# Kernel tuning notes

Measured on AMD Instinct MI355X. Metric: run time of the kernel, lower is better.

The kernel has to match this reference:

```python
import jax, jax.numpy as jnp
import numpy as np


def setup_inputs() -> dict:
    key = jax.random.key(0)
    k1, k2, k3, k4 = jax.random.split(key, 4)
    B, h, w, z, C = 4, 16, 16, 16, 128
    Cq = C // 8
    x = jax.random.normal(k1, (B, h, w, z, C), dtype=jnp.float32)
    # 1x1x1 Conv3D kernels == per-voxel linear projections (he_normal scale)
    Wb = jax.random.normal(k2, (C, Cq), dtype=jnp.float32) * np.sqrt(2.0 / C)
    Wc = jax.random.normal(k3, (C, Cq), dtype=jnp.float32) * np.sqrt(2.0 / C)
    Wd = jax.random.normal(k4, (C, C), dtype=jnp.float32) * np.sqrt(2.0 / C)
    gamma = jnp.zeros((1,), dtype=jnp.float32)
    return {"x": x, "Wb": Wb, "Wc": Wc, "Wd": Wd, "gamma": gamma}


def reference(x, Wb, Wc, Wd, gamma):
    B, h, w, z, C = x.shape
    N = h * w * z
    # 1x1x1 convs = channel projections
    b = jnp.einsum('bhwzc,cf->bhwzf', x, Wb).reshape(B, N, -1)   # [B,N,C/8]
    c = jnp.einsum('bhwzc,cf->bhwzf', x, Wc).reshape(B, N, -1)   # [B,N,C/8]
    d = jnp.einsum('bhwzc,cf->bhwzf', x, Wd).reshape(B, N, C)    # [B,N,C]
    # full NxN attention scores, softmax over last axis (keras softmax default)
    scores = jnp.einsum('bnf,bmf->bnm', b, c)                    # [B,N,N]
    attn = jax.nn.softmax(scores, axis=-1)
    out = jnp.einsum('bnm,bmc->bnc', attn, d).reshape(B, h, w, z, C)
    return gamma * out + x
```

## Files before the change

kernel.cpp:

```cpp
#include <hip/hip_runtime.h>

#define NB     4
#define NN     4096
#define NC     128
#define NCQ    16
#define NROWS  (NB * NN)
#define NSLICE 8
#define NIT    (NN / 64 / NSLICE)

typedef __attribute__((ext_vector_type(8)))  __bf16 bf16x8;
typedef __attribute__((ext_vector_type(4)))  float  f32x4;
typedef __attribute__((ext_vector_type(16))) float  f32x16;

#define MFMA16(a,b,c) __builtin_amdgcn_mfma_f32_16x16x32_bf16((a),(b),(c),0,0,0)
#define MFMA32(a,b,c) __builtin_amdgcn_mfma_f32_32x32x16_bf16((a),(b),(c),0,0,0)
#define LOG2E 1.44269504f
#define SCH_BIAS 16248.66f

__device__ __forceinline__ f32x16 zero16() {
    f32x16 v;
    #pragma unroll
    for (int i = 0; i < 16; ++i) v[i] = 0.f;
    return v;
}


__global__ __launch_bounds__(256) void wpre_kernel(
    const float* __restrict__ Wb, const float* __restrict__ Wc,
    const float* __restrict__ Wd, __bf16* __restrict__ Wp)
{
    int idx = blockIdx.x * 256 + threadIdx.x;
    int oc = idx >> 7, ch = idx & 127;
    float v;
    if (oc < 16)      v = Wb[ch * 16 + oc];
    else if (oc < 32) v = Wc[ch * 16 + (oc - 16)];
    else              v = Wd[ch * 128 + (oc - 32)];
    Wp[idx] = (__bf16)v;
}

__global__ __launch_bounds__(256) void proj_kernel(
    const float* __restrict__ x,  const __bf16* __restrict__ Wp,
    __bf16* __restrict__ qswz, __bf16* __restrict__ kswz,
    __bf16* __restrict__ vswz)
{
    __shared__ __align__(16) __bf16 xsh[32 * 136];
    __shared__ __align__(16) float  osb[4][16 * 17];

    const int  t    = threadIdx.x;
    const int  lane = t & 63, w = t >> 6;
    const int  q16  = lane & 15, quad = lane >> 4;
    const long row0 = (long)blockIdx.x * 32;
    const int  batch = (int)(row0 >> 12);
    const int  nloc  = (int)(row0 & 4095);
    const int  rh   = w & 1;
    const int  og   = (w >> 1) * 5;

    #pragma unroll
    for (int i = 0; i < 4; ++i) {
        int idx = t + 256 * i;
        int r = idx >> 5, c4 = (idx & 31) * 4;
        float4 xv = *(const float4*)&x[(row0 + r) * NC + c4];
        union { __bf16 h[4]; uint2 u; } cv;
        cv.h[0] = (__bf16)xv.x; cv.h[1] = (__bf16)xv.y;
        cv.h[2] = (__bf16)xv.z; cv.h[3] = (__bf16)xv.w;
        *(uint2*)&xsh[r * 136 + c4] = cv.u;
    }
    __syncthreads();

    bf16x8 xf[4];
    #pragma unroll
    for (int kc = 0; kc < 4; ++kc)
        xf[kc] = *(const bf16x8*)&xsh[(rh * 16 + q16) * 136 + kc * 32 + quad * 8];

    const __bf16* wbase = Wp + (size_t)(og * 16 + q16) * 128 + quad * 8;
    bf16x8 wfb[4];
    #pragma unroll
    for (int kc = 0; kc < 4; ++kc)
        wfb[kc] = *(const bf16x8*)(wbase + kc * 32);

    float* osw = osb[w];
    #pragma unroll
    for (int oc_t = 0; oc_t < 5; ++oc_t) {
        const int oset = og + oc_t;
        bf16x8 wfc[4];
        #pragma unroll
        for (int kc = 0; kc < 4; ++kc) wfc[kc] = wfb[kc];
        if (oc_t < 4) {
            const __bf16* wn = wbase + (size_t)(oc_t + 1) * 2048;
            #pragma unroll
            for (int kc = 0; kc < 4; ++kc)
                wfb[kc] = *(const bf16x8*)(wn + kc * 32);
        }
        f32x4 acc = {0.f, 0.f, 0.f, 0.f};
        #pragma unroll
        for (int kc = 0; kc < 4; ++kc)
            acc = MFMA16(wfc[kc], xf[kc], acc);
        #pragma unroll
        for (int r = 0; r < 4; ++r)
            osw[(quad * 4 + r) * 17 + q16] = acc[r];

        if (oset >= 2) {
            int ch_l = lane & 15, lh_t = (lane >> 4) & 1, jh = lane >> 5;
            union { __bf16 h[4]; uint2 u; } cv;
            #pragma unroll
            for (int u2 = 0; u2 < 4; ++u2)
                cv.h[u2] = (__bf16)osw[ch_l * 17 + 8 * jh + 4 * lh_t + u2];
            int kb16 = (nloc >> 4) + rh;
            int cg   = (oset - 2) >> 1;
            int l31v = ((oset - 2) & 1) * 16 + ch_l;
            size_t off = ((((size_t)batch * 256 + kb16) * 4 + cg) << 9)
                       + (size_t)(lh_t * 32 + l31v) * 8 + jh * 4;
            *(uint2*)&vswz[off] = cv.u;
        } else if (lane < 32) {
            int xr = lane & 15, lh_t = lane >> 4;
            const float qsc = (oset == 0) ? LOG2E : 1.f;
            union { __bf16 h[8]; uint4 u; } cv;
            #pragma unroll
            for (int j = 0; j < 8; ++j)
                cv.h[j] = (__bf16)(osw[(8 * lh_t + j) * 17 + xr] * qsc);
            size_t off = ((((size_t)batch * 128 + (nloc >> 5)) * 64)
                       + (size_t)(lh_t * 32 + rh * 16 + xr)) * 8;
            __bf16* dst = (oset == 0) ? qswz : kswz;
            *(uint4*)&dst[off] = cv.u;
        }
    }
}

__global__ __launch_bounds__(256, 4) void attn_kernel(
    const __bf16* __restrict__ qswz, const __bf16* __restrict__ kswz,
    const __bf16* __restrict__ vswz, __bf16* __restrict__ Opart,
    float* __restrict__ lws)
{
    const int t    = threadIdx.x;
    const int lane = t & 63, w = t >> 6;
    const int l31 = lane & 31, lh = lane >> 5;
    const int bid   = blockIdx.x;
    const int xcd   = bid & 7;
    const int batch = xcd >> 1;
    const int spL   = xcd & 1;
    const int idx   = bid >> 3;
    const int qpair = idx & 63;
    const int spH   = idx >> 6;
    const int slice = (spH << 1) | spL;
    const int qb32  = qpair * 2 + (w >> 1);
    const int h     = w & 1;
    const int ks0   = slice * (64 * NIT);

    const bf16x8 qf = *(const bf16x8*)
        &qswz[(((size_t)batch * 128 + qb32) * 64 + lane) * 8];

    const __bf16* kptr = kswz + ((size_t)batch * 128 + (ks0 >> 5)) * 512 + lane * 8;
    const __bf16* vptr = vswz + ((size_t)batch * 256 + (ks0 >> 4)) * 2048
                       + h * 1024 + lane * 8;

    union { uint32_t u[4]; bf16x8 f; } onesu;
    #pragma unroll
    for (int i = 0; i < 4; ++i) onesu.u[i] = 0x3F803F80u;
    const bf16x8 ones = onesu.f;

    f32x16 O0 = zero16(), O1 = zero16(), Ol = zero16();

    bf16x8 kf0 = *(const bf16x8*)(kptr);
    bf16x8 kf1 = *(const bf16x8*)(kptr + 512);
    bf16x8 va[8], vb[8];
    #pragma unroll
    for (int b = 0; b < 4; ++b) {
        va[2*b]     = *(const bf16x8*)(vptr + (size_t)(b * 4)     * 512);
        va[2*b + 1] = *(const bf16x8*)(vptr + (size_t)(b * 4 + 1) * 512);
    }
    f32x16 S0 = MFMA32(kf0, qf, zero16());
    f32x16 S1 = MFMA32(kf1, qf, zero16());

#define ATTN_BODY(IT, CUR, NXT)                                               \
    {                                                                         \
        const int itn = ((IT) + 1 < NIT) ? (IT) + 1 : (IT);                   \
        kf0 = *(const bf16x8*)(kptr + (size_t)itn * 1024);                    \
        kf1 = *(const bf16x8*)(kptr + (size_t)itn * 1024 + 512);              \
        _Pragma("unroll")                                                     \
        for (int b = 0; b < 4; ++b) {                                         \
            NXT[2*b]     = *(const bf16x8*)(vptr + (size_t)((itn*4+b)*4)*512);\
            NXT[2*b + 1] = *(const bf16x8*)(vptr + (size_t)((itn*4+b)*4+1)*512);\
        }                                                                     \
        union { uint32_t u32[16]; bf16x8 f[4]; } pk;                          \
        _Pragma("unroll")                                                     \
        for (int i = 0; i < 8; ++i) {                                         \
            int e0 = (int)fmaf(S0[2*i],   128.f, SCH_BIAS);                   \
            int e1 = (int)fmaf(S0[2*i+1], 128.f, SCH_BIAS);                   \
            int e2 = (int)fmaf(S1[2*i],   128.f, SCH_BIAS);                   \
            int e3 = (int)fmaf(S1[2*i+1], 128.f, SCH_BIAS);                   \
            pk.u32[i]     = (uint32_t)((e1 << 16) | e0);                      \
            pk.u32[8 + i] = (uint32_t)((e3 << 16) | e2);                      \
        }                                                                     \
        _Pragma("unroll")                                                     \
        for (int b = 0; b < 4; ++b) {                                         \
            O0 = MFMA32(pk.f[b], CUR[2*b],     O0);                           \
            O1 = MFMA32(pk.f[b], CUR[2*b + 1], O1);                           \
            Ol = MFMA32(pk.f[b], ones,         Ol);                           \
        }                                                                     \
        S0 = MFMA32(kf0, qf, zero16());                                       \
        S1 = MFMA32(kf1, qf, zero16());                                       \
    }

    for (int it = 0; it < NIT; it += 2) {
        ATTN_BODY(it,     va, vb);
        ATTN_BODY(it + 1, vb, va);
    }
#undef ATTN_BODY

    const long base = (long)batch * NN;

    if (h == 0 && l31 == 0) {
        #pragma unroll
        for (int r = 0; r < 16; ++r) {
            int q = qb32 * 32 + (r & 3) + 8 * (r >> 2) + 4 * lh;
            lws[(size_t)slice * NROWS + base + q] = Ol[r];
        }
    }

    #pragma unroll
    for (int ct = 0; ct < 2; ++ct) {
        f32x16 Ov = ct ? O1 : O0;
        #pragma unroll
        for (int r = 0; r < 16; ++r) {
            int q = qb32 * 32 + (r & 3) + 8 * (r >> 2) + 4 * lh;
            Opart[((size_t)slice * NROWS + base + q) * NC + 64 * h + 32 * ct + l31]
                = (__bf16)Ov[r];
        }
    }
}

__global__ __launch_bounds__(256) void combine_kernel(
    const __bf16* __restrict__ Op, const float* __restrict__ lws,
    const float* __restrict__ x, const float* __restrict__ gamma,
    float* __restrict__ out)
{
    __shared__ float gl[32];
    const int  t    = threadIdx.x;
    const long row0 = (long)blockIdx.x * 32;
    if (t < 32) {
        float l = 0.f;
        #pragma unroll
        for (int s = 0; s < NSLICE; ++s) l += lws[(size_t)s * NROWS + row0 + t];
        gl[t] = gamma[0] / l;
    }
    __syncthreads();
    const size_t s1 = (size_t)NROWS * NC;
    #pragma unroll
    for (int i = 0; i < 2; ++i) {
        int idx = t + 256 * i;
        int r = idx >> 4, c8 = (idx & 15) * 8;
        size_t g = (size_t)(row0 + r) * NC + c8;
        float a[8];
        #pragma unroll
        for (int j = 0; j < 8; ++j) a[j] = 0.f;
        #pragma unroll
        for (int s = 0; s < NSLICE; ++s) {
            union { __bf16 h[8]; uint4 u; } av;
            av.u = *(const uint4*)&Op[s1 * s + g];
            #pragma unroll
            for (int j = 0; j < 8; ++j) a[j] += (float)av.h[j];
        }
        float sc = gl[r];
        float4 x0 = *(const float4*)&x[g];
        float4 x1 = *(const float4*)&x[g + 4];
        float4 o0, o1;
        o0.x = a[0] * sc + x0.x; o0.y = a[1] * sc + x0.y;
        o0.z = a[2] * sc + x0.z; o0.w = a[3] * sc + x0.w;
        o1.x = a[4] * sc + x1.x; o1.y = a[5] * sc + x1.y;
        o1.z = a[6] * sc + x1.z; o1.w = a[7] * sc + x1.w;
        *(float4*)&out[g]     = o0;
        *(float4*)&out[g + 4] = o1;
    }
}

extern "C" void kernel_launch(void* const* d_in, const int* in_sizes, int n_in,
                              void* d_out, int out_size, void* d_ws, size_t ws_size,
                              hipStream_t stream) {
    const float* x     = (const float*)d_in[0];
    const float* Wb    = (const float*)d_in[1];
    const float* Wc    = (const float*)d_in[2];
    const float* Wd    = (const float*)d_in[3];
    const float* gamma = (const float*)d_in[4];
    float*       out   = (float*)d_out;

    __bf16* qswz  = (__bf16*)d_ws;
    __bf16* kswz  = qswz + (size_t)NROWS * NCQ;
    __bf16* vswz  = kswz + (size_t)NROWS * NCQ;
    __bf16* Opart = vswz + (size_t)NB * NC * NN;
    float*  lws   = (float*)(Opart + (size_t)NSLICE * NROWS * NC);
    __bf16* Wp    = (__bf16*)(lws + (size_t)NSLICE * NROWS);

    wpre_kernel   <<<80, 256, 0, stream>>>(Wb, Wc, Wd, Wp);
    proj_kernel   <<<NROWS / 32, 256, 0, stream>>>(x, Wp, qswz, kswz, vswz);
    attn_kernel   <<<NB * 128 * 4, 256, 0, stream>>>(qswz, kswz, vswz, Opart, lws);
    combine_kernel<<<NROWS / 32, 256, 0, stream>>>(Opart, lws, x, gamma, out);
}
```

Baseline: 129.8 us.

## Halve key slices, compute row sums on VALU, stage partial outputs through LDS

The key dimension is now split into 4 slices instead of 8, which halves the grid and the partial-output and row-sum traffic that the combine kernel has to read. The row-sum MFMA against a ones vector is replaced by a scalar accumulation of the bf16-cast exponentials plus a cross-half shuffle. That removes one of every three PV-stage MFMAs. Partial outputs are transposed through shared memory so each block writes them as coalesced 16-byte stores, and the loop is fully unrolled. In exchange, V is no longer prefetched one iteration ahead, so load latency may be exposed, and fewer blocks give less parallelism across the GPU.

```diff
diff --git a/kernel.cpp b/kernel.cpp
--- a/kernel.cpp
+++ b/kernel.cpp
@@ -5,7 +5,7 @@
 #define NC     128
 #define NCQ    16
 #define NROWS  (NB * NN)
-#define NSLICE 8
+#define NSLICE 4
 #define NIT    (NN / 64 / NSLICE)
 
 typedef __attribute__((ext_vector_type(8)))  __bf16 bf16x8;
@@ -131,6 +131,8 @@
     const __bf16* __restrict__ vswz, __bf16* __restrict__ Opart,
     float* __restrict__ lws)
 {
+    __shared__ __align__(16) __bf16 osh[64 * 136];
+
     const int t    = threadIdx.x;
     const int lane = t & 63, w = t >> 6;
     const int l31 = lane & 31, lh = lane >> 5;
@@ -153,33 +155,25 @@
     const __bf16* vptr = vswz + ((size_t)batch * 256 + (ks0 >> 4)) * 2048
                        + h * 1024 + lane * 8;
 
-    union { uint32_t u[4]; bf16x8 f; } onesu;
-    #pragma unroll
-    for (int i = 0; i < 4; ++i) onesu.u[i] = 0x3F803F80u;
-    const bf16x8 ones = onesu.f;
-
-    f32x16 O0 = zero16(), O1 = zero16(), Ol = zero16();
+    f32x16 O0 = zero16(), O1 = zero16();
+    float  lacc = 0.f;
+    const bool do_l = (h == 0);
 
     bf16x8 kf0 = *(const bf16x8*)(kptr);
     bf16x8 kf1 = *(const bf16x8*)(kptr + 512);
-    bf16x8 va[8], vb[8];
-    #pragma unroll
-    for (int b = 0; b < 4; ++b) {
-        va[2*b]     = *(const bf16x8*)(vptr + (size_t)(b * 4)     * 512);
-        va[2*b + 1] = *(const bf16x8*)(vptr + (size_t)(b * 4 + 1) * 512);
-    }
     f32x16 S0 = MFMA32(kf0, qf, zero16());
     f32x16 S1 = MFMA32(kf1, qf, zero16());
 
-#define ATTN_BODY(IT, CUR, NXT)                                               \
+#define ATTN_BODY(IT)                                                         \
     {                                                                         \
         const int itn = ((IT) + 1 < NIT) ? (IT) + 1 : (IT);                   \
         kf0 = *(const bf16x8*)(kptr + (size_t)itn * 1024);                    \
         kf1 = *(const bf16x8*)(kptr + (size_t)itn * 1024 + 512);              \
+        bf16x8 va[8];                                                         \
         _Pragma("unroll")                                                     \
         for (int b = 0; b < 4; ++b) {                                         \
-            NXT[2*b]     = *(const bf16x8*)(vptr + (size_t)((itn*4+b)*4)*512);\
-            NXT[2*b + 1] = *(const bf16x8*)(vptr + (size_t)((itn*4+b)*4+1)*512);\
+            va[2*b]   = *(const bf16x8*)(vptr + (size_t)(((IT)*4+b)*4)*512);  \
+            va[2*b+1] = *(const bf16x8*)(vptr + (size_t)(((IT)*4+b)*4+1)*512);\
         }                                                                     \
         union { uint32_t u32[16]; bf16x8 f[4]; } pk;                          \
         _Pragma("unroll")                                                     \
@@ -190,42 +184,54 @@
             int e3 = (int)fmaf(S1[2*i+1], 128.f, SCH_BIAS);                   \
             pk.u32[i]     = (uint32_t)((e1 << 16) | e0);                      \
             pk.u32[8 + i] = (uint32_t)((e3 << 16) | e2);                      \
+            if (do_l) {                                                       \
+                union { uint32_t u; float fv; } c0, c1, c2, c3;               \
+                c0.u = (uint32_t)e0 << 16; c1.u = (uint32_t)e1 << 16;         \
+                c2.u = (uint32_t)e2 << 16; c3.u = (uint32_t)e3 << 16;         \
+                lacc += (c0.fv + c1.fv) + (c2.fv + c3.fv);                    \
+            }                                                                 \
         }                                                                     \
         _Pragma("unroll")                                                     \
         for (int b = 0; b < 4; ++b) {                                         \
-            O0 = MFMA32(pk.f[b], CUR[2*b],     O0);                           \
-            O1 = MFMA32(pk.f[b], CUR[2*b + 1], O1);                           \
-            Ol = MFMA32(pk.f[b], ones,         Ol);                           \
+            O0 = MFMA32(pk.f[b], va[2*b],     O0);                            \
+            O1 = MFMA32(pk.f[b], va[2*b + 1], O1);                            \
         }                                                                     \
         S0 = MFMA32(kf0, qf, zero16());                                       \
         S1 = MFMA32(kf1, qf, zero16());                                       \
     }
 
+    #pragma unroll
     for (int it = 0; it < NIT; it += 2) {
-        ATTN_BODY(it,     va, vb);
-        ATTN_BODY(it + 1, vb, va);
+        ATTN_BODY(it);
+        ATTN_BODY(it + 1);
     }
 #undef ATTN_BODY
 
     const long base = (long)batch * NN;
-
-    if (h == 0 && l31 == 0) {
-        #pragma unroll
-        for (int r = 0; r < 16; ++r) {
-            int q = qb32 * 32 + (r & 3) + 8 * (r >> 2) + 4 * lh;
-            lws[(size_t)slice * NROWS + base + q] = Ol[r];
-        }
-    }
+    const int  qr0  = (w >> 1) * 32;
+
+    float lfull = lacc + __shfl_xor(lacc, 32);
+    if (h == 0 && lh == 0)
+        lws[(size_t)slice * NROWS + base + qpair * 64 + qr0 + l31] = lfull;
 
     #pragma unroll
     for (int ct = 0; ct < 2; ++ct) {
         f32x16 Ov = ct ? O1 : O0;
         #pragma unroll
         for (int r = 0; r < 16; ++r) {
-            int q = qb32 * 32 + (r & 3) + 8 * (r >> 2) + 4 * lh;
-            Opart[((size_t)slice * NROWS + base + q) * NC + 64 * h + 32 * ct + l31]
-                = (__bf16)Ov[r];
+            int qr = qr0 + (r & 3) + 8 * (r >> 2) + 4 * lh;
+            osh[qr * 136 + 64 * h + 32 * ct + l31] = (__bf16)Ov[r];
         }
+    }
+    __syncthreads();
+
+    const int row = t >> 2, seg = t & 3;
+    const size_t gb = ((size_t)slice * NROWS + base + qpair * 64 + row) * NC
+                    + seg * 32;
+    #pragma unroll
+    for (int k = 0; k < 4; ++k) {
+        uint4 v = *(const uint4*)&osh[row * 136 + seg * 32 + k * 8];
+        *(uint4*)&Opart[gb + k * 8] = v;
     }
 }
 
@@ -292,6 +298,6 @@
 
     wpre_kernel   <<<80, 256, 0, stream>>>(Wb, Wc, Wd, Wp);
     proj_kernel   <<<NROWS / 32, 256, 0, stream>>>(x, Wp, qswz, kswz, vswz);
-    attn_kernel   <<<NB * 128 * 4, 256, 0, stream>>>(qswz, kswz, vswz, Opart, lws);
+    attn_kernel   <<<NB * 64 * NSLICE, 256, 0, stream>>>(qswz, kswz, vswz, Opart, lws);
     combine_kernel<<<NROWS / 32, 256, 0, stream>>>(Opart, lws, x, gamma, out);
 }
```

Result: slower. 158.3 us (+21.9%).
